# Kernel tuning notes

Measured on AMD Instinct MI355X. Metric: run time of the kernel, lower is better.

## Reference

```python
import jax, jax.numpy as jnp
import numpy as np

C = 4096  # d_model (RWKV-7B scale)


def setup_inputs() -> dict:
    key = jax.random.key(0)
    ks = jax.random.split(key, 14)
    vec = lambda k: jax.random.normal(k, (C,), dtype=jnp.float32)
    mat = lambda k: jax.random.normal(k, (C, C), dtype=jnp.float32) * 0.02
    return {
        "x": vec(ks[0]),
        "state": vec(ks[1]),
        "state_a": vec(ks[2]),
        # state_b is a running sum of exponentials in RWKV -> strictly positive
        "state_b": jax.random.uniform(ks[3], (C,), dtype=jnp.float32) + 0.5,
        "state_p": vec(ks[4]),
        "time_mix_k": jax.random.uniform(ks[5], (C,), dtype=jnp.float32),
        "time_mix_v": jax.random.uniform(ks[6], (C,), dtype=jnp.float32),
        "time_mix_r": jax.random.uniform(ks[7], (C,), dtype=jnp.float32),
        "time_first": vec(ks[8]) * 0.5,
        # time_decay is negative in RWKV (exp decay of the state)
        "time_decay": -jnp.abs(vec(ks[9])) - 0.1,
        "kw": mat(ks[10]),
        "vw": mat(ks[11]),
        "rw": mat(ks[12]),
        "ow": mat(ks[13]),
    }


def reference(x, state, state_a, state_b, state_p,
              time_mix_k, time_mix_v, time_mix_r,
              time_first, time_decay, kw, vw, rw, ow):
    # token-shift interpolation with previous token (state)
    xk = x * time_mix_k + state * (1.0 - time_mix_k)
    xv = x * time_mix_v + state * (1.0 - time_mix_v)
    xr = x * time_mix_r + state * (1.0 - time_mix_r)
    new_state = x

    r = jax.nn.sigmoid(rw @ xr)   # [C]
    kk = kw @ xk                  # [C]
    vv = vw @ xv                  # [C]

    aa, bb, pp = state_a, state_b, state_p

    # output accumulators with max-trick stabilization
    ww = time_first + kk
    p = jnp.maximum(pp, ww)
    e1 = jnp.exp(pp - p)
    e2 = jnp.exp(ww - p)
    a = e1 * aa + e2 * vv
    b = e1 * bb + e2

    # state update (decayed accumulators)
    ww = pp + time_decay
    p = jnp.maximum(ww, kk)
    e1 = jnp.exp(ww - p)
    e2 = jnp.exp(kk - p)
    new_state_a = e1 * aa + e2 * vv
    new_state_b = e1 * bb + e2
    new_state_p = p

    wkv = a / b
    out = ow @ (r * wkv)
    return (out, new_state, new_state_a, new_state_b, new_state_p)
```

## Files before the change

kernel.cpp:

```cpp
#include <hip/hip_runtime.h>
#include <math.h>

#define C 4096

__global__ void mix_kernel(const float* __restrict__ x, const float* __restrict__ state,
                           const float* __restrict__ tmk, const float* __restrict__ tmv,
                           const float* __restrict__ tmr,
                           float* __restrict__ xk, float* __restrict__ xv,
                           float* __restrict__ xr, float* __restrict__ new_state) {
    int i = blockIdx.x * blockDim.x + threadIdx.x;
    if (i < C) {
        float xi = x[i], si = state[i];
        float mk = tmk[i], mv = tmv[i], mr = tmr[i];
        xk[i] = xi * mk + si * (1.0f - mk);
        xv[i] = xi * mv + si * (1.0f - mv);
        xr[i] = xi * mr + si * (1.0f - mr);
        new_state[i] = xi;
    }
}

__global__ __launch_bounds__(256) void matvec3_kernel(
    const float* __restrict__ kw, const float* __restrict__ vw, const float* __restrict__ rw,
    const float* __restrict__ xk, const float* __restrict__ xv, const float* __restrict__ xr,
    float* __restrict__ kk, float* __restrict__ vvo, float* __restrict__ rr) {
    int wave = threadIdx.x >> 6;
    int lane = threadIdx.x & 63;
    int row = blockIdx.x * 4 + wave;
    int m = row >> 12;
    int i = row & (C - 1);

    const float* W;
    const float* xin;
    float* out;
    if (m == 0)      { W = kw; xin = xk; out = kk;  }
    else if (m == 1) { W = vw; xin = xv; out = vvo; }
    else             { W = rw; xin = xr; out = rr;  }

    const float4* Wrow = (const float4*)(W + (size_t)i * C);
    const float4* x4   = (const float4*)xin;

    float sum = 0.0f;
#pragma unroll
    for (int it = 0; it < 16; ++it) {
        int idx = it * 64 + lane;
        float4 w  = Wrow[idx];
        float4 xx = x4[idx];
        sum += w.x * xx.x + w.y * xx.y + w.z * xx.z + w.w * xx.w;
    }
#pragma unroll
    for (int off = 32; off > 0; off >>= 1) sum += __shfl_down(sum, off, 64);
    if (lane == 0) out[i] = sum;
}

__global__ void wkv_kernel(const float* __restrict__ kk, const float* __restrict__ vv,
                           const float* __restrict__ rr,
                           const float* __restrict__ aa, const float* __restrict__ bb,
                           const float* __restrict__ pp,
                           const float* __restrict__ time_first,
                           const float* __restrict__ time_decay,
                           float* __restrict__ rwkv,
                           float* __restrict__ out_sa, float* __restrict__ out_sb,
                           float* __restrict__ out_sp) {
    int i = blockIdx.x * blockDim.x + threadIdx.x;
    if (i < C) {
        float k = kk[i], v = vv[i];
        float a_ = aa[i], b_ = bb[i], p_ = pp[i];

        float ww = time_first[i] + k;
        float p  = fmaxf(p_, ww);
        float e1 = expf(p_ - p);
        float e2 = expf(ww - p);
        float a  = e1 * a_ + e2 * v;
        float b  = e1 * b_ + e2;

        float ww2 = p_ + time_decay[i];
        float p2  = fmaxf(ww2, k);
        float e1b = expf(ww2 - p2);
        float e2b = expf(k - p2);
        out_sa[i] = e1b * a_ + e2b * v;
        out_sb[i] = e1b * b_ + e2b;
        out_sp[i] = p2;

        float r = 1.0f / (1.0f + expf(-rr[i]));
        rwkv[i] = r * (a / b);
    }
}

__global__ __launch_bounds__(256) void matvec_kernel(const float* __restrict__ W,
                                                     const float* __restrict__ xin,
                                                     float* __restrict__ out) {
    int wave = threadIdx.x >> 6;
    int lane = threadIdx.x & 63;
    int i = blockIdx.x * 4 + wave;

    const float4* Wrow = (const float4*)(W + (size_t)i * C);
    const float4* x4   = (const float4*)xin;

    float sum = 0.0f;
#pragma unroll
    for (int it = 0; it < 16; ++it) {
        int idx = it * 64 + lane;
        float4 w  = Wrow[idx];
        float4 xx = x4[idx];
        sum += w.x * xx.x + w.y * xx.y + w.z * xx.z + w.w * xx.w;
    }
#pragma unroll
    for (int off = 32; off > 0; off >>= 1) sum += __shfl_down(sum, off, 64);
    if (lane == 0) out[i] = sum;
}

extern "C" void kernel_launch(void* const* d_in, const int* in_sizes, int n_in,
                              void* d_out, int out_size, void* d_ws, size_t ws_size,
                              hipStream_t stream) {
    const float* x          = (const float*)d_in[0];
    const float* state      = (const float*)d_in[1];
    const float* state_a    = (const float*)d_in[2];
    const float* state_b    = (const float*)d_in[3];
    const float* state_p    = (const float*)d_in[4];
    const float* tmk        = (const float*)d_in[5];
    const float* tmv        = (const float*)d_in[6];
    const float* tmr        = (const float*)d_in[7];
    const float* time_first = (const float*)d_in[8];
    const float* time_decay = (const float*)d_in[9];
    const float* kw         = (const float*)d_in[10];
    const float* vw         = (const float*)d_in[11];
    const float* rw         = (const float*)d_in[12];
    const float* ow         = (const float*)d_in[13];

    float* out       = (float*)d_out;
    float* new_state = out + C;
    float* new_sa    = out + 2 * C;
    float* new_sb    = out + 3 * C;
    float* new_sp    = out + 4 * C;

    float* ws   = (float*)d_ws;
    float* xk   = ws;
    float* xv   = ws + C;
    float* xr   = ws + 2 * C;
    float* kk   = ws + 3 * C;
    float* vv   = ws + 4 * C;
    float* rr   = ws + 5 * C;
    float* rwkv = ws + 6 * C;

    mix_kernel<<<C / 256, 256, 0, stream>>>(x, state, tmk, tmv, tmr, xk, xv, xr, new_state);

    matvec3_kernel<<<3 * C / 4, 256, 0, stream>>>(kw, vw, rw, xk, xv, xr, kk, vv, rr);

    wkv_kernel<<<C / 256, 256, 0, stream>>>(kk, vv, rr, state_a, state_b, state_p,
                                            time_first, time_decay,
                                            rwkv, new_sa, new_sb, new_sp);

    matvec_kernel<<<C / 4, 256, 0, stream>>>(ow, rwkv, out);
}
```

Measured before the change: 260.3 us.

## Fuse token-shift mix into matvec, stage input vector in LDS, prefetch weight rows

Removes the separate mix kernel: each matvec3 block now computes its mixed input vector into shared memory directly from x, state and the mix coefficients, and the new_state copy moves into the wkv kernel. Both matvec kernels stage the input vector in LDS, issue all 16 weight float4 loads up front into registers, and split the accumulation across four partial sums. This drops one launch and the intermediate round trip through global memory, at the cost of every block recomputing the 16 KB mix and higher register pressure from the 16 float4 weight registers.

```diff
diff --git a/kernel.cpp b/kernel.cpp
--- a/kernel.cpp
+++ b/kernel.cpp
@@ -3,53 +3,62 @@
 
 #define C 4096
 
-__global__ void mix_kernel(const float* __restrict__ x, const float* __restrict__ state,
-                           const float* __restrict__ tmk, const float* __restrict__ tmv,
-                           const float* __restrict__ tmr,
-                           float* __restrict__ xk, float* __restrict__ xv,
-                           float* __restrict__ xr, float* __restrict__ new_state) {
-    int i = blockIdx.x * blockDim.x + threadIdx.x;
-    if (i < C) {
-        float xi = x[i], si = state[i];
-        float mk = tmk[i], mv = tmv[i], mr = tmr[i];
-        xk[i] = xi * mk + si * (1.0f - mk);
-        xv[i] = xi * mv + si * (1.0f - mv);
-        xr[i] = xi * mr + si * (1.0f - mr);
-        new_state[i] = xi;
-    }
-}
-
 __global__ __launch_bounds__(256) void matvec3_kernel(
     const float* __restrict__ kw, const float* __restrict__ vw, const float* __restrict__ rw,
-    const float* __restrict__ xk, const float* __restrict__ xv, const float* __restrict__ xr,
+    const float* __restrict__ x, const float* __restrict__ state,
+    const float* __restrict__ tmk, const float* __restrict__ tmv, const float* __restrict__ tmr,
     float* __restrict__ kk, float* __restrict__ vvo, float* __restrict__ rr) {
-    int wave = threadIdx.x >> 6;
-    int lane = threadIdx.x & 63;
-    int row = blockIdx.x * 4 + wave;
-    int m = row >> 12;
-    int i = row & (C - 1);
+    __shared__ float4 xs[C / 4];
+
+    const int t = threadIdx.x;
+    const int m = blockIdx.x >> 10;
 
     const float* W;
-    const float* xin;
+    const float* tm;
     float* out;
-    if (m == 0)      { W = kw; xin = xk; out = kk;  }
-    else if (m == 1) { W = vw; xin = xv; out = vvo; }
-    else             { W = rw; xin = xr; out = rr;  }
+    if (m == 0)      { W = kw; tm = tmk; out = kk;  }
+    else if (m == 1) { W = vw; tm = tmv; out = vvo; }
+    else             { W = rw; tm = tmr; out = rr;  }
 
-    const float4* Wrow = (const float4*)(W + (size_t)i * C);
-    const float4* x4   = (const float4*)xin;
+    const float4* x4 = (const float4*)x;
+    const float4* s4 = (const float4*)state;
+    const float4* t4 = (const float4*)tm;
+#pragma unroll
+    for (int j = 0; j < 4; ++j) {
+        int i = j * 256 + t;
+        float4 xi = x4[i], si = s4[i], ti = t4[i];
+        float4 r;
+        r.x = xi.x * ti.x + si.x * (1.0f - ti.x);
+        r.y = xi.y * ti.y + si.y * (1.0f - ti.y);
+        r.z = xi.z * ti.z + si.z * (1.0f - ti.z);
+        r.w = xi.w * ti.w + si.w * (1.0f - ti.w);
+        xs[i] = r;
+    }
+    __syncthreads();
 
-    float sum = 0.0f;
+    const int wave = t >> 6;
+    const int lane = t & 63;
+    const int row  = (blockIdx.x & 1023) * 4 + wave;
+    const float4* Wrow = (const float4*)(W + (size_t)row * C);
+
+    float4 wreg[16];
+#pragma unroll
+    for (int it = 0; it < 16; ++it) wreg[it] = Wrow[it * 64 + lane];
+
+    float s0 = 0.f, s1 = 0.f, s2 = 0.f, s3 = 0.f;
 #pragma unroll
     for (int it = 0; it < 16; ++it) {
-        int idx = it * 64 + lane;
-        float4 w  = Wrow[idx];
-        float4 xx = x4[idx];
-        sum += w.x * xx.x + w.y * xx.y + w.z * xx.z + w.w * xx.w;
+        float4 xx = xs[it * 64 + lane];
+        float4 w  = wreg[it];
+        s0 += w.x * xx.x;
+        s1 += w.y * xx.y;
+        s2 += w.z * xx.z;
+        s3 += w.w * xx.w;
     }
+    float sum = (s0 + s1) + (s2 + s3);
 #pragma unroll
     for (int off = 32; off > 0; off >>= 1) sum += __shfl_down(sum, off, 64);
-    if (lane == 0) out[i] = sum;
+    if (lane == 0) out[row] = sum;
 }
 
 __global__ void wkv_kernel(const float* __restrict__ kk, const float* __restrict__ vv,
@@ -58,7 +67,9 @@
                            const float* __restrict__ pp,
                            const float* __restrict__ time_first,
                            const float* __restrict__ time_decay,
+                           const float* __restrict__ x,
                            float* __restrict__ rwkv,
+                           float* __restrict__ new_state,
                            float* __restrict__ out_sa, float* __restrict__ out_sb,
                            float* __restrict__ out_sp) {
     int i = blockIdx.x * blockDim.x + threadIdx.x;
@@ -81,6 +92,8 @@
         out_sb[i] = e1b * b_ + e2b;
         out_sp[i] = p2;
 
+        new_state[i] = x[i];
+
         float r = 1.0f / (1.0f + expf(-rr[i]));
         rwkv[i] = r * (a / b);
     }
@@ -89,24 +102,40 @@
 __global__ __launch_bounds__(256) void matvec_kernel(const float* __restrict__ W,
                                                      const float* __restrict__ xin,
                                                      float* __restrict__ out) {
-    int wave = threadIdx.x >> 6;
-    int lane = threadIdx.x & 63;
-    int i = blockIdx.x * 4 + wave;
+    __shared__ float4 xs[C / 4];
+    const int t = threadIdx.x;
 
-    const float4* Wrow = (const float4*)(W + (size_t)i * C);
-    const float4* x4   = (const float4*)xin;
+    const float4* x4 = (const float4*)xin;
+#pragma unroll
+    for (int j = 0; j < 4; ++j) {
+        int i = j * 256 + t;
+        xs[i] = x4[i];
+    }
+    __syncthreads();
 
-    float sum = 0.0f;
+    const int wave = t >> 6;
+    const int lane = t & 63;
+    const int row  = blockIdx.x * 4 + wave;
+    const float4* Wrow = (const float4*)(W + (size_t)row * C);
+
+    float4 wreg[16];
+#pragma unroll
+    for (int it = 0; it < 16; ++it) wreg[it] = Wrow[it * 64 + lane];
+
+    float s0 = 0.f, s1 = 0.f, s2 = 0.f, s3 = 0.f;
 #pragma unroll
     for (int it = 0; it < 16; ++it) {
-        int idx = it * 64 + lane;
-        float4 w  = Wrow[idx];
-        float4 xx = x4[idx];
-        sum += w.x * xx.x + w.y * xx.y + w.z * xx.z + w.w * xx.w;
+        float4 xx = xs[it * 64 + lane];
+        float4 w  = wreg[it];
+        s0 += w.x * xx.x;
+        s1 += w.y * xx.y;
+        s2 += w.z * xx.z;
+        s3 += w.w * xx.w;
     }
+    float sum = (s0 + s1) + (s2 + s3);
 #pragma unroll
     for (int off = 32; off > 0; off >>= 1) sum += __shfl_down(sum, off, 64);
-    if (lane == 0) out[i] = sum;
+    if (lane == 0) out[row] = sum;
 }
 
 extern "C" void kernel_launch(void* const* d_in, const int* in_sizes, int n_in,
@@ -134,21 +163,17 @@
     float* new_sp    = out + 4 * C;
 
     float* ws   = (float*)d_ws;
-    float* xk   = ws;
-    float* xv   = ws + C;
-    float* xr   = ws + 2 * C;
-    float* kk   = ws + 3 * C;
-    float* vv   = ws + 4 * C;
-    float* rr   = ws + 5 * C;
-    float* rwkv = ws + 6 * C;
+    float* kk   = ws;
+    float* vv   = ws + C;
+    float* rr   = ws + 2 * C;
+    float* rwkv = ws + 3 * C;
 
-    mix_kernel<<<C / 256, 256, 0, stream>>>(x, state, tmk, tmv, tmr, xk, xv, xr, new_state);
-
-    matvec3_kernel<<<3 * C / 4, 256, 0, stream>>>(kw, vw, rw, xk, xv, xr, kk, vv, rr);
+    matvec3_kernel<<<3 * C / 4, 256, 0, stream>>>(kw, vw, rw, x, state, tmk, tmv, tmr,
+                                                  kk, vv, rr);
 
     wkv_kernel<<<C / 256, 256, 0, stream>>>(kk, vv, rr, state_a, state_b, state_p,
-                                            time_first, time_decay,
-                                            rwkv, new_sa, new_sb, new_sp);
+                                            time_first, time_decay, x,
+                                            rwkv, new_state, new_sa, new_sb, new_sp);
 
     matvec_kernel<<<C / 4, 256, 0, stream>>>(ow, rwkv, out);
 }
```

Result: no change. 258.0 us (-0.9%).
